# Performance work log

Hardware: AMD Instinct MI355X
Metric: run time of the kernel (lower is better)

Reference implementation:

```python
import jax, jax.numpy as jnp
import numpy as np

V, H, L, B, S = 32000, 1024, 2, 8, 256


def setup_inputs() -> dict:
    key = jax.random.key(0)
    ks = jax.random.split(key, 12)
    s = 1.0 / np.sqrt(H)  # PyTorch LSTM/Linear init range
    u = lambda k, shape: jax.random.uniform(k, shape, jnp.float32, -s, s)
    return {
        "x": jax.random.randint(ks[0], (B, S), 0, V, dtype=jnp.int32),
        "h0": jnp.zeros((L, B, H), jnp.float32),
        "c0": jnp.zeros((L, B, H), jnp.float32),
        "w_ih0": u(ks[1], (4 * H, V)),
        "w_hh0": u(ks[2], (4 * H, H)),
        "b_ih0": u(ks[3], (4 * H,)),
        "b_hh0": u(ks[4], (4 * H,)),
        "w_ih1": u(ks[5], (4 * H, H)),
        "w_hh1": u(ks[6], (4 * H, H)),
        "b_ih1": u(ks[7], (4 * H,)),
        "b_hh1": u(ks[8], (4 * H,)),
        "fc_w": u(ks[9], (V, H)),
        "fc_b": u(ks[10], (V,)),
    }


def _lstm_layer(xproj, h0, c0, w_hh):
    """xproj: [S,B,4H] input-to-gate projection (biases folded in).
    Gate order i,f,g,o matches PyTorch."""
    def step(carry, xp):
        h, c = carry
        g = xp + h @ w_hh.T  # [B,4H]
        i, f, gg, o = jnp.split(g, 4, axis=-1)
        c = jax.nn.sigmoid(f) * c + jax.nn.sigmoid(i) * jnp.tanh(gg)
        h = jax.nn.sigmoid(o) * jnp.tanh(c)
        return (h, c), h
    (hT, cT), hs = jax.lax.scan(step, (h0, c0), xproj)
    return hs, hT, cT


def reference(x, h0, c0, w_ih0, w_hh0, b_ih0, b_hh0, w_ih1, w_hh1, b_ih1, b_hh1, fc_w, fc_b):
    # F.one_hot(x, V).float() @ w_ih0.T  ==  gather of rows of w_ih0.T (identical math)
    xp0 = jnp.take(w_ih0.T, x, axis=0) + (b_ih0 + b_hh0)  # [B,S,4H]
    xp0 = xp0.transpose(1, 0, 2)  # [S,B,4H] for time-major scan
    h1s, h1T, c1T = _lstm_layer(xp0, h0[0], c0[0], w_hh0)
    xp1 = h1s @ w_ih1.T + (b_ih1 + b_hh1)  # [S,B,4H]
    h2s, h2T, c2T = _lstm_layer(xp1, h0[1], c0[1], w_hh1)
    out = h2s.transpose(1, 0, 2).reshape(-1, H)  # [B*S,H]
    logits = out @ fc_w.T + fc_b  # [B*S,V]
    hn = jnp.stack([h1T, h2T])
    cn = jnp.stack([c1T, c2T])
    return logits, (hn, cn)
```

## Files before the change

### kernel.cpp

```cpp
#include <hip/hip_runtime.h>
#include <cmath>

typedef float  f32x4  __attribute__((ext_vector_type(4)));
typedef float  f32x2  __attribute__((ext_vector_type(2)));
typedef __bf16 bf16x8 __attribute__((ext_vector_type(8)));

static constexpr int HN  = 1024;
static constexpr int VN  = 32000;
static constexpr int BN  = 8;
static constexpr int SN  = 256;
static constexpr int H4N = 4096;

__global__ __launch_bounds__(256) void k_gather(const int* __restrict__ x,
    const float* __restrict__ w_ih0, const float* __restrict__ b_ih0,
    const float* __restrict__ b_hh0, float* __restrict__ xp) {
  int bid = blockIdx.x;
  int t = bid >> 3, b = bid & 7;
  int tok = x[b * SN + t];
  const float* col = w_ih0 + tok;
  float* dst = xp + (size_t)bid * H4N;
  for (int r = threadIdx.x; r < H4N; r += 256)
    dst[r] = col[(size_t)r * VN] + b_ih0[r] + b_hh0[r];
}

__global__ __launch_bounds__(256, 1) void k_lstm(
    const float* __restrict__ xp,
    const float* __restrict__ w_hh,
    const float* __restrict__ h0,
    const float* __restrict__ c0,
    float* __restrict__ hs,
    float* __restrict__ hn, float* __restrict__ cn,
    unsigned* __restrict__ bar) {
  __shared__ float wL[16][1024];
  __shared__ float hL[8192];
  __shared__ float red[8][4][4][32];
  __shared__ float gates[16][8];
  __shared__ float cL[32];

  const int tid = threadIdx.x;
  const int wg  = blockIdx.x;
  const int u0  = wg * 4;

  for (int it = 0; it < 16; ++it) {
    int g = it >> 2, u = it & 3;
    int k4 = tid;
    int k4s = k4 ^ ((k4 >> 3) & 7);
    f32x4 v = *(const f32x4*)&w_hh[((size_t)g * HN + u0 + u) * HN + k4 * 4];
    *(f32x4*)&wL[it][k4s * 4] = v;
  }
  if (tid < 32) cL[tid] = c0[(tid & 7) * HN + u0 + (tid >> 3)];

  const int ks = tid & 31, rg = (tid >> 5) & 3, bg = tid >> 7;
  const int ksx = ks & 7;
  const int hb = tid & 7;
  const int hk = tid >> 3;

  for (int t = 0; t < SN; ++t) {
    const float* hsrc = (t == 0) ? h0 : (hs + (size_t)(t - 1) * (BN * HN));
    const unsigned long long* hsrc8 =
        (const unsigned long long*)hsrc + (size_t)hb * 512 + hk;
    unsigned long long rv[16];
    #pragma unroll
    for (int j = 0; j < 16; ++j)
      rv[j] = __hip_atomic_load((unsigned long long*)(hsrc8 + j * 32),
                                __ATOMIC_RELAXED, __HIP_MEMORY_SCOPE_AGENT);
    #pragma unroll
    for (int j = 0; j < 16; ++j) {
      int k64 = hk + j * 32;
      int k4 = k64 >> 1, half = k64 & 1;
      int idx = ((k4 << 3) | hb) ^ ((k4 >> 3) & 7);
      *(f32x2*)&hL[idx * 4 + half * 2] = __builtin_bit_cast(f32x2, rv[j]);
    }
    __syncthreads();

    float acc[4][4] = {};
    #pragma unroll
    for (int j = 0; j < 8; ++j) {
      int k4 = ks * 8 + j;
      int k4s = k4 ^ ksx;
      f32x4 wv[4], hv[4];
      #pragma unroll
      for (int ri = 0; ri < 4; ++ri)
        wv[ri] = *(const f32x4*)&wL[rg * 4 + ri][k4s * 4];
      #pragma unroll
      for (int bi = 0; bi < 4; ++bi) {
        int idx = ((k4 << 3) | (bg * 4 + bi)) ^ ksx;
        hv[bi] = *(const f32x4*)&hL[idx * 4];
      }
      #pragma unroll
      for (int ri = 0; ri < 4; ++ri)
        #pragma unroll
        for (int bi = 0; bi < 4; ++bi)
          acc[ri][bi] += wv[ri][0]*hv[bi][0] + wv[ri][1]*hv[bi][1]
                       + wv[ri][2]*hv[bi][2] + wv[ri][3]*hv[bi][3];
    }
    #pragma unroll
    for (int ri = 0; ri < 4; ++ri)
      #pragma unroll
      for (int bi = 0; bi < 4; ++bi)
        red[rg * 2 + bg][ri][bi][ks] = acc[ri][bi];
    __syncthreads();

    if (tid < 128) {
      int row = tid >> 3, b = tid & 7;
      int rrg = row >> 2, ri = row & 3, bbg = b >> 2, bi = b & 3;
      const float* rp = red[rrg * 2 + bbg][ri][bi];
      float s = 0.f;
      #pragma unroll
      for (int q = 0; q < 32; ++q) s += rp[(q + tid) & 31];
      int g = row >> 2, u = row & 3;
      s += xp[(size_t)t * (BN * H4N) + b * H4N + g * HN + u0 + u];
      gates[row][b] = s;
    }
    __syncthreads();

    if (tid < 32) {
      int u = tid >> 3, b = tid & 7;
      float gi = gates[0 * 4 + u][b], gf = gates[1 * 4 + u][b];
      float gg = gates[2 * 4 + u][b], go = gates[3 * 4 + u][b];
      float si = 1.f / (1.f + expf(-gi));
      float sf = 1.f / (1.f + expf(-gf));
      float so = 1.f / (1.f + expf(-go));
      float c = sf * cL[tid] + si * tanhf(gg);
      float h = so * tanhf(c);
      cL[tid] = c;
      __hip_atomic_store(&hs[(size_t)t * (BN * HN) + b * HN + u0 + u], h,
                         __ATOMIC_RELAXED, __HIP_MEMORY_SCOPE_AGENT);
      if (t == SN - 1) {
        hn[b * HN + u0 + u] = h;
        cn[b * HN + u0 + u] = c;
      }
    }

    if (t != SN - 1) {
      if (tid == 0) {
        asm volatile("s_waitcnt vmcnt(0)" ::: "memory");
        __hip_atomic_fetch_add(&bar[(wg >> 2) * 32], 1u,
                               __ATOMIC_RELAXED, __HIP_MEMORY_SCOPE_AGENT);
      }
      if (tid < 64) {
        unsigned tgt = 4u * (unsigned)(t + 1);
        while (__hip_atomic_load(&bar[tid * 32], __ATOMIC_RELAXED,
                                 __HIP_MEMORY_SCOPE_AGENT) < tgt)
          __builtin_amdgcn_s_sleep(1);
      }
      __syncthreads();
    } else {
      __syncthreads();
    }
  }
}

__global__ __launch_bounds__(256) void k_split(const float* __restrict__ src,
    __bf16* __restrict__ hi, __bf16* __restrict__ lo) {
  int i = (blockIdx.x * 256 + threadIdx.x) * 4;
  f32x4 v = *(const f32x4*)&src[i];
  #pragma unroll
  for (int j = 0; j < 4; ++j) {
    __bf16 h = (__bf16)v[j];
    hi[i + j] = h;
    lo[i + j] = (__bf16)(v[j] - (float)h);
  }
}

__global__ __launch_bounds__(256) void k_gemm(const __bf16* __restrict__ Ahi,
    const __bf16* __restrict__ Alo, const float* __restrict__ Bsrc,
    const float* __restrict__ bias1, const float* __restrict__ bias2,
    float* __restrict__ C, int Mt, int N, int permute) {
  __shared__ __bf16 sAh[128][32], sAl[128][32], sBh[128][32], sBl[128][32];
  int bid = blockIdx.x;
  int tn = bid / Mt, tm = bid % Mt;
  int tid = threadIdx.x, lane = tid & 63, wid = tid >> 6;
  int wr = wid >> 1, wc = wid & 1;
  f32x4 acc[4][4] = {};
  const size_t K = 1024;

  for (int kk = 0; kk < 1024; kk += 32) {
    __syncthreads();
    #pragma unroll
    for (int it = 0; it < 2; ++it) {
      int c = it * 256 + tid;
      int r = c >> 2, k8 = (c & 3) * 8;
      size_t ga = (size_t)(tm * 128 + r) * K + kk + k8;
      *(bf16x8*)&sAh[r][k8] = *(const bf16x8*)&Ahi[ga];
      *(bf16x8*)&sAl[r][k8] = *(const bf16x8*)&Alo[ga];
      size_t gb = (size_t)(tn * 128 + r) * K + kk + k8;
      f32x4 x0 = *(const f32x4*)&Bsrc[gb];
      f32x4 x1 = *(const f32x4*)&Bsrc[gb + 4];
      bf16x8 bh, bl;
      #pragma unroll
      for (int j = 0; j < 4; ++j) {
        __bf16 h0 = (__bf16)x0[j]; bh[j]     = h0; bl[j]     = (__bf16)(x0[j] - (float)h0);
        __bf16 h1 = (__bf16)x1[j]; bh[4 + j] = h1; bl[4 + j] = (__bf16)(x1[j] - (float)h1);
      }
      *(bf16x8*)&sBh[r][k8] = bh;
      *(bf16x8*)&sBl[r][k8] = bl;
    }
    __syncthreads();

    int kq = (lane >> 4) * 8;
    bf16x8 ah[4], al[4], bh[4], bl[4];
    #pragma unroll
    for (int i = 0; i < 4; ++i) {
      int ra = wr * 64 + i * 16 + (lane & 15);
      ah[i] = *(const bf16x8*)&sAh[ra][kq];
      al[i] = *(const bf16x8*)&sAl[ra][kq];
      int rb = wc * 64 + i * 16 + (lane & 15);
      bh[i] = *(const bf16x8*)&sBh[rb][kq];
      bl[i] = *(const bf16x8*)&sBl[rb][kq];
    }
    #pragma unroll
    for (int i = 0; i < 4; ++i)
      #pragma unroll
      for (int j = 0; j < 4; ++j) {
        acc[i][j] = __builtin_amdgcn_mfma_f32_16x16x32_bf16(ah[i], bh[j], acc[i][j], 0, 0, 0);
        acc[i][j] = __builtin_amdgcn_mfma_f32_16x16x32_bf16(ah[i], bl[j], acc[i][j], 0, 0, 0);
        acc[i][j] = __builtin_amdgcn_mfma_f32_16x16x32_bf16(al[i], bh[j], acc[i][j], 0, 0, 0);
      }
  }

  #pragma unroll
  for (int j = 0; j < 4; ++j) {
    int gcol = tn * 128 + wc * 64 + j * 16 + (lane & 15);
    float bv = bias1[gcol] + (bias2 ? bias2[gcol] : 0.f);
    #pragma unroll
    for (int i = 0; i < 4; ++i) {
      #pragma unroll
      for (int r = 0; r < 4; ++r) {
        int row = tm * 128 + wr * 64 + i * 16 + ((lane >> 4) << 2) + r;
        int orow = permute ? ((row & 7) * 256 + (row >> 3)) : row;
        C[(size_t)orow * N + gcol] = acc[i][j][r] + bv;
      }
    }
  }
}

extern "C" void kernel_launch(void* const* d_in, const int* in_sizes, int n_in,
                              void* d_out, int out_size, void* d_ws, size_t ws_size,
                              hipStream_t stream) {
  (void)in_sizes; (void)n_in; (void)out_size; (void)ws_size;
  const int*   x     = (const int*)  d_in[0];
  const float* h0    = (const float*)d_in[1];
  const float* c0    = (const float*)d_in[2];
  const float* w_ih0 = (const float*)d_in[3];
  const float* w_hh0 = (const float*)d_in[4];
  const float* b_ih0 = (const float*)d_in[5];
  const float* b_hh0 = (const float*)d_in[6];
  const float* w_ih1 = (const float*)d_in[7];
  const float* w_hh1 = (const float*)d_in[8];
  const float* b_ih1 = (const float*)d_in[9];
  const float* b_hh1 = (const float*)d_in[10];
  const float* fc_w  = (const float*)d_in[11];
  const float* fc_b  = (const float*)d_in[12];
  float* out = (float*)d_out;
  float* ws  = (float*)d_ws;

  float* xp   = ws;
  float* h1s  = ws + 8388608;
  float* h2s  = ws + 10485760;
  __bf16* Ahi = (__bf16*)(ws + 12582912);
  __bf16* Alo = (__bf16*)(ws + 13631488);
  unsigned* bar = (unsigned*)(ws + 14680064);

  const size_t LOG = (size_t)2048 * VN;
  float* hn = out + LOG;
  float* cn = out + LOG + 16384;

  hipMemsetAsync(bar, 0, 4096 * sizeof(unsigned), stream);

  k_gather<<<SN * BN, 256, 0, stream>>>(x, w_ih0, b_ih0, b_hh0, xp);

  k_lstm<<<256, 256, 0, stream>>>(xp, w_hh0, h0, c0, h1s, hn, cn, bar);

  k_split<<<2048, 256, 0, stream>>>(h1s, Ahi, Alo);
  k_gemm<<<16 * 32, 256, 0, stream>>>(Ahi, Alo, w_ih1, b_ih1, b_hh1, xp,
                                      16, H4N, 0);

  k_lstm<<<256, 256, 0, stream>>>(xp, w_hh1, h0 + BN * HN, c0 + BN * HN,
                                  h2s, hn + BN * HN, cn + BN * HN, bar + 2048);

  k_split<<<2048, 256, 0, stream>>>(h2s, Ahi, Alo);
  k_gemm<<<16 * 250, 256, 0, stream>>>(Ahi, Alo, fc_w, fc_b, nullptr, out,
                                       16, VN, 1);
}
```

Measured before the change: 4.246 ms.

## Fuse both LSTM layers into one wavefront-pipelined persistent kernel

Replaces the two sequential persistent LSTM kernels, the layer-1 input-projection GEMM and its split kernel with a single persistent kernel. In that kernel, step s computes layer 1 at time s and layer 2 at time s-1, so one grid barrier per step serves both layers. Layer-2 input projection is computed on the fly from w_ih1 read through global memory/cache, and w_hh0 and w_hh1 are both held in LDS. This halves the number of serial barrier steps and removes the middle GEMM, but each step does roughly three times the matvec work and streams w_ih1 from cache every step.

```diff
diff --git a/kernel.cpp b/kernel.cpp
--- a/kernel.cpp
+++ b/kernel.cpp
@@ -23,19 +23,22 @@
     dst[r] = col[(size_t)r * VN] + b_ih0[r] + b_hh0[r];
 }
 
-__global__ __launch_bounds__(256, 1) void k_lstm(
-    const float* __restrict__ xp,
-    const float* __restrict__ w_hh,
+__global__ __launch_bounds__(256, 1) void k_lstm2(
+    const float* __restrict__ xp0,
+    const float* __restrict__ w_hh0,
+    const float* __restrict__ w_ih1,
+    const float* __restrict__ w_hh1,
+    const float* __restrict__ bi1,
+    const float* __restrict__ bh1,
     const float* __restrict__ h0,
     const float* __restrict__ c0,
-    float* __restrict__ hs,
+    float* __restrict__ h1s,
+    float* __restrict__ h2s,
     float* __restrict__ hn, float* __restrict__ cn,
     unsigned* __restrict__ bar) {
-  __shared__ float wL[16][1024];
+  __shared__ float wL0[16][1024];
+  __shared__ float wL1[16][1024];
   __shared__ float hL[8192];
-  __shared__ float red[8][4][4][32];
-  __shared__ float gates[16][8];
-  __shared__ float cL[32];
 
   const int tid = threadIdx.x;
   const int wg  = blockIdx.x;
@@ -45,108 +48,206 @@
     int g = it >> 2, u = it & 3;
     int k4 = tid;
     int k4s = k4 ^ ((k4 >> 3) & 7);
-    f32x4 v = *(const f32x4*)&w_hh[((size_t)g * HN + u0 + u) * HN + k4 * 4];
-    *(f32x4*)&wL[it][k4s * 4] = v;
-  }
-  if (tid < 32) cL[tid] = c0[(tid & 7) * HN + u0 + (tid >> 3)];
+    *(f32x4*)&wL0[it][k4s * 4] =
+        *(const f32x4*)&w_hh0[((size_t)g * HN + u0 + u) * HN + k4 * 4];
+    *(f32x4*)&wL1[it][k4s * 4] =
+        *(const f32x4*)&w_hh1[((size_t)g * HN + u0 + u) * HN + k4 * 4];
+  }
+  float c1 = 0.f, c2 = 0.f;
+  if (tid < 32) c1 = c0[(tid & 7) * HN + u0 + (tid >> 3)];
+  else if (tid < 64) {
+    int l = tid - 32;
+    c2 = c0[BN * HN + (l & 7) * HN + u0 + (l >> 3)];
+  }
 
   const int ks = tid & 31, rg = (tid >> 5) & 3, bg = tid >> 7;
   const int ksx = ks & 7;
-  const int hb = tid & 7;
-  const int hk = tid >> 3;
-
-  for (int t = 0; t < SN; ++t) {
-    const float* hsrc = (t == 0) ? h0 : (hs + (size_t)(t - 1) * (BN * HN));
-    const unsigned long long* hsrc8 =
-        (const unsigned long long*)hsrc + (size_t)hb * 512 + hk;
-    unsigned long long rv[16];
-    #pragma unroll
-    for (int j = 0; j < 16; ++j)
-      rv[j] = __hip_atomic_load((unsigned long long*)(hsrc8 + j * 32),
-                                __ATOMIC_RELAXED, __HIP_MEMORY_SCOPE_AGENT);
+  const int hb = tid & 7, hk = tid >> 3;
+
+  const int prow = (tid & 127) >> 3, pb = tid & 7;
+  const int pg = prow >> 2, pu = prow & 3;
+  const int grow = pg * HN + u0 + pu;
+  float bsum1 = 0.f;
+  if (tid >= 128) bsum1 = bi1[grow] + bh1[grow];
+  const float* wih1_t = w_ih1 + ((size_t)rg * HN + u0) * HN + ks * 32;
+  __syncthreads();
+
+  for (int s = 0; s <= SN; ++s) {
+    float xpv = 0.f;
+    if (s < SN && tid < 128)
+      xpv = xp0[(size_t)s * (BN * H4N) + (size_t)pb * H4N + grow];
+
+    if (s > 0) {
+      if (tid < 64) {
+        unsigned tgt = 4u * (unsigned)s;
+        while (__hip_atomic_load(&bar[tid * 32], __ATOMIC_RELAXED,
+                                 __HIP_MEMORY_SCOPE_AGENT) < tgt)
+          __builtin_amdgcn_s_sleep(1);
+      }
+      __syncthreads();
+    }
+
+    unsigned long long rv1[16], rv2[16];
+    if (s == 0) {
+      const unsigned long long* p =
+          (const unsigned long long*)h0 + (size_t)hb * 512 + hk;
+      #pragma unroll
+      for (int j = 0; j < 16; ++j) rv1[j] = p[j * 32];
+    } else {
+      const unsigned long long* p =
+          (const unsigned long long*)(h1s + (size_t)(s - 1) * (BN * HN))
+          + (size_t)hb * 512 + hk;
+      #pragma unroll
+      for (int j = 0; j < 16; ++j)
+        rv1[j] = __hip_atomic_load((unsigned long long*)(p + j * 32),
+                                   __ATOMIC_RELAXED, __HIP_MEMORY_SCOPE_AGENT);
+      if (s == 1) {
+        const unsigned long long* q =
+            (const unsigned long long*)(h0 + BN * HN) + (size_t)hb * 512 + hk;
+        #pragma unroll
+        for (int j = 0; j < 16; ++j) rv2[j] = q[j * 32];
+      } else {
+        const unsigned long long* q =
+            (const unsigned long long*)(h2s + (size_t)(s - 2) * (BN * HN))
+            + (size_t)hb * 512 + hk;
+        #pragma unroll
+        for (int j = 0; j < 16; ++j)
+          rv2[j] = __hip_atomic_load((unsigned long long*)(q + j * 32),
+                                     __ATOMIC_RELAXED, __HIP_MEMORY_SCOPE_AGENT);
+      }
+    }
+
     #pragma unroll
     for (int j = 0; j < 16; ++j) {
-      int k64 = hk + j * 32;
-      int k4 = k64 >> 1, half = k64 & 1;
+      int k64 = hk + j * 32, k4 = k64 >> 1, half = k64 & 1;
       int idx = ((k4 << 3) | hb) ^ ((k4 >> 3) & 7);
-      *(f32x2*)&hL[idx * 4 + half * 2] = __builtin_bit_cast(f32x2, rv[j]);
-    }
-    __syncthreads();
-
-    float acc[4][4] = {};
+      *(f32x2*)&hL[idx * 4 + half * 2] = __builtin_bit_cast(f32x2, rv1[j]);
+    }
+    __syncthreads();
+
+    float acc1[4][4] = {}, acc2[4][4] = {};
     #pragma unroll
     for (int j = 0; j < 8; ++j) {
       int k4 = ks * 8 + j;
       int k4s = k4 ^ ksx;
-      f32x4 wv[4], hv[4];
-      #pragma unroll
-      for (int ri = 0; ri < 4; ++ri)
-        wv[ri] = *(const f32x4*)&wL[rg * 4 + ri][k4s * 4];
-      #pragma unroll
-      for (int bi = 0; bi < 4; ++bi) {
-        int idx = ((k4 << 3) | (bg * 4 + bi)) ^ ksx;
-        hv[bi] = *(const f32x4*)&hL[idx * 4];
-      }
-      #pragma unroll
-      for (int ri = 0; ri < 4; ++ri)
-        #pragma unroll
-        for (int bi = 0; bi < 4; ++bi)
-          acc[ri][bi] += wv[ri][0]*hv[bi][0] + wv[ri][1]*hv[bi][1]
-                       + wv[ri][2]*hv[bi][2] + wv[ri][3]*hv[bi][3];
-    }
+      f32x4 hv[4];
+      #pragma unroll
+      for (int b2 = 0; b2 < 4; ++b2)
+        hv[b2] = *(const f32x4*)&hL[(((k4 << 3) | (bg * 4 + b2)) ^ ksx) * 4];
+      if (s < SN) {
+        #pragma unroll
+        for (int ri = 0; ri < 4; ++ri) {
+          f32x4 wv = *(const f32x4*)&wL0[rg * 4 + ri][k4s * 4];
+          #pragma unroll
+          for (int b2 = 0; b2 < 4; ++b2)
+            acc1[ri][b2] += wv[0]*hv[b2][0] + wv[1]*hv[b2][1]
+                          + wv[2]*hv[b2][2] + wv[3]*hv[b2][3];
+        }
+      }
+      if (s > 0) {
+        #pragma unroll
+        for (int ri = 0; ri < 4; ++ri) {
+          f32x4 wv = *(const f32x4*)&wih1_t[(size_t)ri * HN + j * 4];
+          #pragma unroll
+          for (int b2 = 0; b2 < 4; ++b2)
+            acc2[ri][b2] += wv[0]*hv[b2][0] + wv[1]*hv[b2][1]
+                          + wv[2]*hv[b2][2] + wv[3]*hv[b2][3];
+        }
+      }
+    }
+
+    if (s > 0) {
+      __syncthreads();
+      #pragma unroll
+      for (int j = 0; j < 16; ++j) {
+        int k64 = hk + j * 32, k4 = k64 >> 1, half = k64 & 1;
+        int idx = ((k4 << 3) | hb) ^ ((k4 >> 3) & 7);
+        *(f32x2*)&hL[idx * 4 + half * 2] = __builtin_bit_cast(f32x2, rv2[j]);
+      }
+      __syncthreads();
+      #pragma unroll
+      for (int j = 0; j < 8; ++j) {
+        int k4 = ks * 8 + j;
+        int k4s = k4 ^ ksx;
+        f32x4 hv[4];
+        #pragma unroll
+        for (int b2 = 0; b2 < 4; ++b2)
+          hv[b2] = *(const f32x4*)&hL[(((k4 << 3) | (bg * 4 + b2)) ^ ksx) * 4];
+        #pragma unroll
+        for (int ri = 0; ri < 4; ++ri) {
+          f32x4 wv = *(const f32x4*)&wL1[rg * 4 + ri][k4s * 4];
+          #pragma unroll
+          for (int b2 = 0; b2 < 4; ++b2)
+            acc2[ri][b2] += wv[0]*hv[b2][0] + wv[1]*hv[b2][1]
+                          + wv[2]*hv[b2][2] + wv[3]*hv[b2][3];
+        }
+      }
+    }
+    __syncthreads();
+
     #pragma unroll
     for (int ri = 0; ri < 4; ++ri)
       #pragma unroll
-      for (int bi = 0; bi < 4; ++bi)
-        red[rg * 2 + bg][ri][bi][ks] = acc[ri][bi];
-    __syncthreads();
-
-    if (tid < 128) {
-      int row = tid >> 3, b = tid & 7;
-      int rrg = row >> 2, ri = row & 3, bbg = b >> 2, bi = b & 3;
-      const float* rp = red[rrg * 2 + bbg][ri][bi];
-      float s = 0.f;
-      #pragma unroll
-      for (int q = 0; q < 32; ++q) s += rp[(q + tid) & 31];
-      int g = row >> 2, u = row & 3;
-      s += xp[(size_t)t * (BN * H4N) + b * H4N + g * HN + u0 + u];
-      gates[row][b] = s;
-    }
-    __syncthreads();
-
-    if (tid < 32) {
+      for (int b2 = 0; b2 < 4; ++b2) {
+        int fo = ((((rg * 2 + bg) * 4 + ri) * 4 + b2) << 5) + ks;
+        hL[fo]        = acc1[ri][b2];
+        hL[4096 + fo] = acc2[ri][b2];
+      }
+    __syncthreads();
+
+    {
+      int fo = ((((prow >> 2) * 2 + (pb >> 2)) * 4 + (prow & 3)) * 4
+                + (pb & 3)) << 5;
+      float* R = (tid < 128) ? hL : (hL + 4096);
+      float sv = 0.f;
+      #pragma unroll
+      for (int q = 0; q < 32; ++q) sv += R[fo + ((q + tid) & 31)];
+      sv += (tid < 128) ? xpv : bsum1;
+      R[fo] = sv;
+    }
+    __syncthreads();
+
+    if (s < SN && tid < 32) {
       int u = tid >> 3, b = tid & 7;
-      float gi = gates[0 * 4 + u][b], gf = gates[1 * 4 + u][b];
-      float gg = gates[2 * 4 + u][b], go = gates[3 * 4 + u][b];
-      float si = 1.f / (1.f + expf(-gi));
-      float sf = 1.f / (1.f + expf(-gf));
-      float so = 1.f / (1.f + expf(-go));
-      float c = sf * cL[tid] + si * tanhf(gg);
-      float h = so * tanhf(c);
-      cL[tid] = c;
-      __hip_atomic_store(&hs[(size_t)t * (BN * HN) + b * HN + u0 + u], h,
+      float gv[4];
+      #pragma unroll
+      for (int g = 0; g < 4; ++g)
+        gv[g] = hL[(((g * 2 + (b >> 2)) * 4 + u) * 4 + (b & 3)) << 5];
+      float si = 1.f / (1.f + expf(-gv[0]));
+      float sf = 1.f / (1.f + expf(-gv[1]));
+      float so = 1.f / (1.f + expf(-gv[3]));
+      c1 = sf * c1 + si * tanhf(gv[2]);
+      float h = so * tanhf(c1);
+      __hip_atomic_store(&h1s[(size_t)s * (BN * HN) + b * HN + u0 + u], h,
                          __ATOMIC_RELAXED, __HIP_MEMORY_SCOPE_AGENT);
-      if (t == SN - 1) {
+      if (s == SN - 1) {
         hn[b * HN + u0 + u] = h;
-        cn[b * HN + u0 + u] = c;
-      }
-    }
-
-    if (t != SN - 1) {
-      if (tid == 0) {
-        asm volatile("s_waitcnt vmcnt(0)" ::: "memory");
-        __hip_atomic_fetch_add(&bar[(wg >> 2) * 32], 1u,
-                               __ATOMIC_RELAXED, __HIP_MEMORY_SCOPE_AGENT);
-      }
-      if (tid < 64) {
-        unsigned tgt = 4u * (unsigned)(t + 1);
-        while (__hip_atomic_load(&bar[tid * 32], __ATOMIC_RELAXED,
-                                 __HIP_MEMORY_SCOPE_AGENT) < tgt)
-          __builtin_amdgcn_s_sleep(1);
-      }
-      __syncthreads();
-    } else {
-      __syncthreads();
+        cn[b * HN + u0 + u] = c1;
+      }
+    }
+    if (s > 0 && tid >= 32 && tid < 64) {
+      int l = tid - 32, u = l >> 3, b = l & 7;
+      float gv[4];
+      #pragma unroll
+      for (int g = 0; g < 4; ++g)
+        gv[g] = hL[4096 + ((((g * 2 + (b >> 2)) * 4 + u) * 4 + (b & 3)) << 5)];
+      float si = 1.f / (1.f + expf(-gv[0]));
+      float sf = 1.f / (1.f + expf(-gv[1]));
+      float so = 1.f / (1.f + expf(-gv[3]));
+      c2 = sf * c2 + si * tanhf(gv[2]);
+      float h = so * tanhf(c2);
+      __hip_atomic_store(&h2s[(size_t)(s - 1) * (BN * HN) + b * HN + u0 + u],
+                         h, __ATOMIC_RELAXED, __HIP_MEMORY_SCOPE_AGENT);
+      if (s == SN) {
+        hn[BN * HN + b * HN + u0 + u] = h;
+        cn[BN * HN + b * HN + u0 + u] = c2;
+      }
+    }
+
+    if (s < SN && tid == 0) {
+      asm volatile("s_waitcnt vmcnt(0)" ::: "memory");
+      __hip_atomic_fetch_add(&bar[(wg >> 2) * 32], 1u,
+                             __ATOMIC_RELAXED, __HIP_MEMORY_SCOPE_AGENT);
     }
   }
 }
@@ -255,7 +356,7 @@
   float* out = (float*)d_out;
   float* ws  = (float*)d_ws;
 
-  float* xp   = ws;
+  float* xp0  = ws;
   float* h1s  = ws + 8388608;
   float* h2s  = ws + 10485760;
   __bf16* Ahi = (__bf16*)(ws + 12582912);
@@ -266,18 +367,12 @@
   float* hn = out + LOG;
   float* cn = out + LOG + 16384;
 
-  hipMemsetAsync(bar, 0, 4096 * sizeof(unsigned), stream);
-
-  k_gather<<<SN * BN, 256, 0, stream>>>(x, w_ih0, b_ih0, b_hh0, xp);
-
-  k_lstm<<<256, 256, 0, stream>>>(xp, w_hh0, h0, c0, h1s, hn, cn, bar);
-
-  k_split<<<2048, 256, 0, stream>>>(h1s, Ahi, Alo);
-  k_gemm<<<16 * 32, 256, 0, stream>>>(Ahi, Alo, w_ih1, b_ih1, b_hh1, xp,
-                                      16, H4N, 0);
-
-  k_lstm<<<256, 256, 0, stream>>>(xp, w_hh1, h0 + BN * HN, c0 + BN * HN,
-                                  h2s, hn + BN * HN, cn + BN * HN, bar + 2048);
+  hipMemsetAsync(bar, 0, 2048 * sizeof(unsigned), stream);
+
+  k_gather<<<SN * BN, 256, 0, stream>>>(x, w_ih0, b_ih0, b_hh0, xp0);
+
+  k_lstm2<<<256, 256, 0, stream>>>(xp0, w_hh0, w_ih1, w_hh1, b_ih1, b_hh1,
+                                   h0, c0, h1s, h2s, hn, cn, bar);
 
   k_split<<<2048, 256, 0, stream>>>(h2s, Ahi, Alo);
   k_gemm<<<16 * 250, 256, 0, stream>>>(Ahi, Alo, fc_w, fc_b, nullptr, out,
```

Result: slower. 5.011 ms (+18.0%).

## Block xproj layout per workgroup, shuffle-reduce gates, and prefetch before barrier wait

Applied to the files above, without the earlier changes.

Stores the input-to-gate projection in a per-workgroup blocked layout, written by both the gather kernel and the layer-1 GEMM epilogue, so each LSTM step reads one contiguous 128-float chunk. The xproj load is issued before the grid-barrier spin. The LDS partial-sum reduction pass is replaced with warp xor-shuffles, and the cell state moves to a register. The gather kernel now runs one block per timestep with coalesced stores. This aims to shorten the per-step serial critical path, at the cost of more shuffle instructions and a scattered write pattern in the GEMM epilogue.

```diff
diff --git a/kernel.cpp b/kernel.cpp
--- a/kernel.cpp
+++ b/kernel.cpp
@@ -13,18 +13,33 @@
 
 __global__ __launch_bounds__(256) void k_gather(const int* __restrict__ x,
     const float* __restrict__ w_ih0, const float* __restrict__ b_ih0,
-    const float* __restrict__ b_hh0, float* __restrict__ xp) {
-  int bid = blockIdx.x;
-  int t = bid >> 3, b = bid & 7;
-  int tok = x[b * SN + t];
-  const float* col = w_ih0 + tok;
-  float* dst = xp + (size_t)bid * H4N;
-  for (int r = threadIdx.x; r < H4N; r += 256)
-    dst[r] = col[(size_t)r * VN] + b_ih0[r] + b_hh0[r];
+    const float* __restrict__ b_hh0, float* __restrict__ xpB) {
+  int t = blockIdx.x;
+  __shared__ int toks[8];
+  if (threadIdx.x < 8) toks[threadIdx.x] = x[threadIdx.x * SN + t];
+  __syncthreads();
+  int wgx = threadIdx.x;
+  for (int g = 0; g < 4; ++g) {
+    float vals[4][8];
+    #pragma unroll
+    for (int u = 0; u < 4; ++u) {
+      int row = g * 1024 + wgx * 4 + u;
+      float bias = b_ih0[row] + b_hh0[row];
+      const float* wr = w_ih0 + (size_t)row * VN;
+      #pragma unroll
+      for (int b = 0; b < 8; ++b) vals[u][b] = wr[toks[b]] + bias;
+    }
+    float* dst = xpB + (((size_t)t * 256 + wgx) * 16 + g * 4) * 8;
+    #pragma unroll
+    for (int u = 0; u < 4; ++u) {
+      *(f32x4*)&dst[u * 8]     = *(f32x4*)&vals[u][0];
+      *(f32x4*)&dst[u * 8 + 4] = *(f32x4*)&vals[u][4];
+    }
+  }
 }
 
 __global__ __launch_bounds__(256, 1) void k_lstm(
-    const float* __restrict__ xp,
+    const float* __restrict__ xpB,
     const float* __restrict__ w_hh,
     const float* __restrict__ h0,
     const float* __restrict__ c0,
@@ -33,9 +48,7 @@
     unsigned* __restrict__ bar) {
   __shared__ float wL[16][1024];
   __shared__ float hL[8192];
-  __shared__ float red[8][4][4][32];
   __shared__ float gates[16][8];
-  __shared__ float cL[32];
 
   const int tid = threadIdx.x;
   const int wg  = blockIdx.x;
@@ -48,22 +61,46 @@
     f32x4 v = *(const f32x4*)&w_hh[((size_t)g * HN + u0 + u) * HN + k4 * 4];
     *(f32x4*)&wL[it][k4s * 4] = v;
   }
-  if (tid < 32) cL[tid] = c0[(tid & 7) * HN + u0 + (tid >> 3)];
+  float c_reg = 0.f;
+  if (tid < 32) c_reg = c0[(tid & 7) * HN + u0 + (tid >> 3)];
 
   const int ks = tid & 31, rg = (tid >> 5) & 3, bg = tid >> 7;
   const int ksx = ks & 7;
   const int hb = tid & 7;
   const int hk = tid >> 3;
+  const int ku = ks >> 2, kb = ks & 3;
+  const int lrow = rg * 4 + ku, lb = bg * 4 + kb;
+  __syncthreads();
 
   for (int t = 0; t < SN; ++t) {
-    const float* hsrc = (t == 0) ? h0 : (hs + (size_t)(t - 1) * (BN * HN));
-    const unsigned long long* hsrc8 =
-        (const unsigned long long*)hsrc + (size_t)hb * 512 + hk;
+    float xpv = 0.f;
+    if (ks < 16) xpv = xpB[((size_t)t * 256 + wg) * 128 + lrow * 8 + lb];
+
+    if (t > 0) {
+      if (tid < 64) {
+        unsigned tgt = 4u * (unsigned)t;
+        while (__hip_atomic_load(&bar[tid * 32], __ATOMIC_RELAXED,
+                                 __HIP_MEMORY_SCOPE_AGENT) < tgt)
+          __builtin_amdgcn_s_sleep(1);
+      }
+      __syncthreads();
+    }
+
     unsigned long long rv[16];
-    #pragma unroll
-    for (int j = 0; j < 16; ++j)
-      rv[j] = __hip_atomic_load((unsigned long long*)(hsrc8 + j * 32),
-                                __ATOMIC_RELAXED, __HIP_MEMORY_SCOPE_AGENT);
+    if (t == 0) {
+      const unsigned long long* s8 =
+          (const unsigned long long*)h0 + (size_t)hb * 512 + hk;
+      #pragma unroll
+      for (int j = 0; j < 16; ++j) rv[j] = s8[j * 32];
+    } else {
+      const unsigned long long* hsrc8 =
+          (const unsigned long long*)(hs + (size_t)(t - 1) * (BN * HN))
+          + (size_t)hb * 512 + hk;
+      #pragma unroll
+      for (int j = 0; j < 16; ++j)
+        rv[j] = __hip_atomic_load((unsigned long long*)(hsrc8 + j * 32),
+                                  __ATOMIC_RELAXED, __HIP_MEMORY_SCOPE_AGENT);
+    }
     #pragma unroll
     for (int j = 0; j < 16; ++j) {
       int k64 = hk + j * 32;
@@ -94,24 +131,16 @@
           acc[ri][bi] += wv[ri][0]*hv[bi][0] + wv[ri][1]*hv[bi][1]
                        + wv[ri][2]*hv[bi][2] + wv[ri][3]*hv[bi][3];
     }
-    #pragma unroll
-    for (int ri = 0; ri < 4; ++ri)
-      #pragma unroll
-      for (int bi = 0; bi < 4; ++bi)
-        red[rg * 2 + bg][ri][bi][ks] = acc[ri][bi];
-    __syncthreads();
-
-    if (tid < 128) {
-      int row = tid >> 3, b = tid & 7;
-      int rrg = row >> 2, ri = row & 3, bbg = b >> 2, bi = b & 3;
-      const float* rp = red[rrg * 2 + bbg][ri][bi];
-      float s = 0.f;
-      #pragma unroll
-      for (int q = 0; q < 32; ++q) s += rp[(q + tid) & 31];
-      int g = row >> 2, u = row & 3;
-      s += xp[(size_t)t * (BN * H4N) + b * H4N + g * HN + u0 + u];
-      gates[row][b] = s;
-    }
+
+    #pragma unroll
+    for (int m = 1; m <= 16; m <<= 1)
+      #pragma unroll
+      for (int ri = 0; ri < 4; ++ri)
+        #pragma unroll
+        for (int bi = 0; bi < 4; ++bi)
+          acc[ri][bi] += __shfl_xor(acc[ri][bi], m);
+
+    if (ks < 16) gates[lrow][lb] = acc[ku][kb] + xpv;
     __syncthreads();
 
     if (tid < 32) {
@@ -121,14 +150,13 @@
       float si = 1.f / (1.f + expf(-gi));
       float sf = 1.f / (1.f + expf(-gf));
       float so = 1.f / (1.f + expf(-go));
-      float c = sf * cL[tid] + si * tanhf(gg);
-      float h = so * tanhf(c);
-      cL[tid] = c;
+      c_reg = sf * c_reg + si * tanhf(gg);
+      float h = so * tanhf(c_reg);
       __hip_atomic_store(&hs[(size_t)t * (BN * HN) + b * HN + u0 + u], h,
                          __ATOMIC_RELAXED, __HIP_MEMORY_SCOPE_AGENT);
       if (t == SN - 1) {
         hn[b * HN + u0 + u] = h;
-        cn[b * HN + u0 + u] = c;
+        cn[b * HN + u0 + u] = c_reg;
       }
     }
 
@@ -137,12 +165,6 @@
         asm volatile("s_waitcnt vmcnt(0)" ::: "memory");
         __hip_atomic_fetch_add(&bar[(wg >> 2) * 32], 1u,
                                __ATOMIC_RELAXED, __HIP_MEMORY_SCOPE_AGENT);
-      }
-      if (tid < 64) {
-        unsigned tgt = 4u * (unsigned)(t + 1);
-        while (__hip_atomic_load(&bar[tid * 32], __ATOMIC_RELAXED,
-                                 __HIP_MEMORY_SCOPE_AGENT) < tgt)
-          __builtin_amdgcn_s_sleep(1);
       }
       __syncthreads();
     } else {
@@ -166,7 +188,7 @@
 __global__ __launch_bounds__(256) void k_gemm(const __bf16* __restrict__ Ahi,
     const __bf16* __restrict__ Alo, const float* __restrict__ Bsrc,
     const float* __restrict__ bias1, const float* __restrict__ bias2,
-    float* __restrict__ C, int Mt, int N, int permute) {
+    float* __restrict__ C, int Mt, int N, int mode) {
   __shared__ __bf16 sAh[128][32], sAl[128][32], sBh[128][32], sBl[128][32];
   int bid = blockIdx.x;
   int tn = bid / Mt, tm = bid % Mt;
@@ -228,8 +250,15 @@
       #pragma unroll
       for (int r = 0; r < 4; ++r) {
         int row = tm * 128 + wr * 64 + i * 16 + ((lane >> 4) << 2) + r;
-        int orow = permute ? ((row & 7) * 256 + (row >> 3)) : row;
-        C[(size_t)orow * N + gcol] = acc[i][j][r] + bv;
+        float val = acc[i][j][r] + bv;
+        if (mode == 2) {
+          int t = row >> 3, b = row & 7;
+          int g = gcol >> 10, rem = gcol & 1023, wgx = rem >> 2, u = rem & 3;
+          C[(((size_t)t * 256 + wgx) * 16 + g * 4 + u) * 8 + b] = val;
+        } else {
+          int orow = (mode == 1) ? ((row & 7) * 256 + (row >> 3)) : row;
+          C[(size_t)orow * N + gcol] = val;
+        }
       }
     }
   }
@@ -255,7 +284,7 @@
   float* out = (float*)d_out;
   float* ws  = (float*)d_ws;
 
-  float* xp   = ws;
+  float* xpB  = ws;
   float* h1s  = ws + 8388608;
   float* h2s  = ws + 10485760;
   __bf16* Ahi = (__bf16*)(ws + 12582912);
@@ -268,15 +297,15 @@
 
   hipMemsetAsync(bar, 0, 4096 * sizeof(unsigned), stream);
 
-  k_gather<<<SN * BN, 256, 0, stream>>>(x, w_ih0, b_ih0, b_hh0, xp);
-
-  k_lstm<<<256, 256, 0, stream>>>(xp, w_hh0, h0, c0, h1s, hn, cn, bar);
+  k_gather<<<SN, 256, 0, stream>>>(x, w_ih0, b_ih0, b_hh0, xpB);
+
+  k_lstm<<<256, 256, 0, stream>>>(xpB, w_hh0, h0, c0, h1s, hn, cn, bar);
 
   k_split<<<2048, 256, 0, stream>>>(h1s, Ahi, Alo);
-  k_gemm<<<16 * 32, 256, 0, stream>>>(Ahi, Alo, w_ih1, b_ih1, b_hh1, xp,
-                                      16, H4N, 0);
-
-  k_lstm<<<256, 256, 0, stream>>>(xp, w_hh1, h0 + BN * HN, c0 + BN * HN,
+  k_gemm<<<16 * 32, 256, 0, stream>>>(Ahi, Alo, w_ih1, b_ih1, b_hh1, xpB,
+                                      16, H4N, 2);
+
+  k_lstm<<<256, 256, 0, stream>>>(xpB, w_hh1, h0 + BN * HN, c0 + BN * HN,
                                   h2s, hn + BN * HN, cn + BN * HN, bar + 2048);
 
   k_split<<<2048, 256, 0, stream>>>(h2s, Ahi, Alo);
```

Result: slower. 5.261 ms (+23.9%).
